# Performance work log

Hardware: AMD Instinct MI355X
Metric: run time of the kernel (lower is better)

Reference implementation:

```python
import jax, jax.numpy as jnp
import numpy as np
import math

NUM_REG_TOKENS = 0  # encoder.num_register_tokens
EPS = 1e-12         # matches torch F.normalize eps


def _l2norm(x):
    # F.normalize(x, dim=-1): x / max(||x||, eps)
    n = jnp.sqrt(jnp.sum(x * x, axis=-1, keepdims=True))
    return x / jnp.maximum(n, EPS)


def setup_inputs() -> dict:
    key = jax.random.key(0)
    k1, k2 = jax.random.split(key)
    L, N, S, T, D = 3, 8, 4, 1370, 768  # 3 interested layers, T = 1 + 37^2 patches
    q_feats = jax.random.normal(k1, (L, N, T, D), dtype=jnp.float32)
    s_feats = jax.random.normal(k2, (L, N * S, T, D), dtype=jnp.float32)
    return {"q_feats": q_feats, "s_feats": s_feats}


def reference(q_feats, s_feats):
    # fuse_feature: mean over stacked interested layers
    xq = jnp.mean(q_feats, axis=0)   # [N, T, D]
    xs = jnp.mean(s_feats, axis=0)   # [N*S, T, D]
    N = xq.shape[0]
    Q = xq.shape[1] - 1 - NUM_REG_TOKENS
    side = int(math.isqrt(Q))
    # drop class (+register) tokens
    xq = xq[:, 1 + NUM_REG_TOKENS:, :]                 # [N, Q, D]
    xs = xs[:, 1 + NUM_REG_TOKENS:, :]                 # [N*S, Q, D]
    xs = xs.reshape(N, -1, xs.shape[-1])               # [N, S*Q, D]
    xq = _l2norm(xq)
    xs = _l2norm(xs)
    # cosine distance + 1-NN min over support tokens
    sim = jnp.einsum('nqd,nsd->nqs', xq, xs)           # [N, Q, S*Q]
    dist = jnp.min(1.0 - sim, axis=-1)                 # [N, Q]
    return dist.reshape(N, 1, side, side)
```

## Files before the change

### kernel.cpp

```cpp
#include <hip/hip_runtime.h>
#include <hip/hip_bf16.h>

typedef __attribute__((ext_vector_type(16))) float f32x16;
typedef __attribute__((ext_vector_type(8))) int i32x8;

#define T_TOK 1370
#define DDIM  768
#define SCV   1369
#define SCP   1408
#define MQP   1536
#define NB    8
#define NSLAB 32
#define NST   44
#define NMT   6

#define MEMFENCE asm volatile("" ::: "memory")
#define BARRIER  do { __builtin_amdgcn_s_barrier(); MEMFENCE; } while (0)

#define GLOAD_LDS16(g, l)                                                     \
  __builtin_amdgcn_global_load_lds(                                           \
      (const __attribute__((address_space(1))) unsigned int*)(g),             \
      (__attribute__((address_space(3))) unsigned int*)(l), 16, 0, 0)

extern "C" __global__ __launch_bounds__(192) void prep_kernel(
    const float* __restrict__ src, unsigned char* __restrict__ dst,
    size_t lstride)
{
  const int row  = blockIdx.x;
  const int slab = blockIdx.y;
  const int t    = threadIdx.x;
  unsigned char* drow = dst + ((size_t)slab * gridDim.x + row) * DDIM;
  if (row >= SCV) {
    reinterpret_cast<unsigned int*>(drow)[t] = 0u;
    return;
  }
  const float* base = src + ((size_t)slab * T_TOK + row + 1) * DDIM;
  float4 a = reinterpret_cast<const float4*>(base)[t];
  float4 b = reinterpret_cast<const float4*>(base + lstride)[t];
  float4 c = reinterpret_cast<const float4*>(base + 2 * lstride)[t];
  const float k3 = 1.0f / 3.0f;
  float4 m;
  m.x = (a.x + b.x + c.x) * k3;
  m.y = (a.y + b.y + c.y) * k3;
  m.z = (a.z + b.z + c.z) * k3;
  m.w = (a.w + b.w + c.w) * k3;
  float ss = m.x * m.x + m.y * m.y + m.z * m.z + m.w * m.w;
  #pragma unroll
  for (int d = 1; d < 64; d <<= 1) ss += __shfl_xor(ss, d);
  __shared__ float wsum[3];
  if ((t & 63) == 0) wsum[t >> 6] = ss;
  __syncthreads();
  float tot = wsum[0] + wsum[1] + wsum[2];
  float rn = 1.0f / fmaxf(sqrtf(tot), 1e-12f);
  int pk = __builtin_amdgcn_cvt_pk_fp8_f32(m.x * rn, m.y * rn, 0, false);
  pk = __builtin_amdgcn_cvt_pk_fp8_f32(m.z * rn, m.w * rn, pk, true);
  reinterpret_cast<unsigned int*>(drow)[t] = (unsigned int)pk;
}

extern "C" __global__ __launch_bounds__(256, 2) void simmax_kernel(
    const unsigned char* __restrict__ xq,
    const unsigned char* __restrict__ xs,
    float* __restrict__ part)
{
  const int flat = blockIdx.x + NMT * (blockIdx.y + NST * blockIdx.z);
  const int swz  = (flat & 7) * (NMT * NST) + (flat >> 3);
  const int mt   = swz % NMT;
  const int st   = (swz / NMT) % NST;
  const int n    = swz / (NMT * NST);

  const int tid  = threadIdx.x;
  const int lane = tid & 63;
  const int w    = tid >> 6;
  const int wr   = w >> 1;
  const int wc   = w & 1;
  const int l31  = lane & 31;
  const int h    = lane >> 5;

  __shared__ unsigned char ring[3][24576];

  const int slab = st / 11;
  const int lt   = st - slab * 11;
  const unsigned char* gA = xq + ((size_t)n * MQP + (size_t)mt * 256) * DDIM;
  const unsigned char* gB =
      xs + ((size_t)(n * 4 + slab) * SCP + (size_t)lt * 128) * DDIM;

  int aoffg[4], aldso[4], boffg[2], bldso[2];
  #pragma unroll
  for (int i = 0; i < 4; ++i) {
    int c = w * 4 + i;
    int r = c * 16 + (lane >> 2);
    aoffg[i] = r * DDIM + (((lane & 3) ^ (r & 3)) << 4);
    aldso[i] = c * 1024;
  }
  #pragma unroll
  for (int i = 0; i < 2; ++i) {
    int c = w * 2 + i;
    int r = c * 16 + (lane >> 2);
    boffg[i] = r * DDIM + (((lane & 3) ^ (r & 3)) << 4);
    bldso[i] = 16384 + c * 1024;
  }

  int aoff[4], boff[2];
  #pragma unroll
  for (int mf = 0; mf < 4; ++mf) {
    int row = wr * 128 + mf * 32 + l31;
    aoff[mf] = row * 64 + ((((h << 1) ^ (row & 3))) << 4);
  }
  #pragma unroll
  for (int nf = 0; nf < 2; ++nf) {
    int row = wc * 64 + nf * 32 + l31;
    boff[nf] = 16384 + row * 64 + ((((h << 1) ^ (row & 3))) << 4);
  }

  f32x16 acc[4][2];
  {
    f32x16 zz = {0.f,0.f,0.f,0.f,0.f,0.f,0.f,0.f,
                 0.f,0.f,0.f,0.f,0.f,0.f,0.f,0.f};
    #pragma unroll
    for (int a = 0; a < 4; ++a)
      #pragma unroll
      for (int b = 0; b < 2; ++b) acc[a][b] = zz;
  }

  #define ISSUE(KT, RB)                                                      \
    do {                                                                     \
      const unsigned char* ga_ = gA + (KT) * 64;                             \
      const unsigned char* gb_ = gB + (KT) * 64;                             \
      unsigned char* lb_ = ring[RB];                                         \
      _Pragma("unroll") for (int i = 0; i < 4; ++i)                          \
        GLOAD_LDS16(ga_ + aoffg[i], lb_ + aldso[i]);                         \
      _Pragma("unroll") for (int i = 0; i < 2; ++i)                          \
        GLOAD_LDS16(gb_ + boffg[i], lb_ + bldso[i]);                         \
    } while (0)

  ISSUE(0, 0);
  ISSUE(1, 1);
  asm volatile("s_waitcnt vmcnt(6)" ::: "memory");
  BARRIER;

  for (int kt = 0; kt < 12; ++kt) {
    if (kt + 2 < 12) ISSUE(kt + 2, (kt + 2) % 3);

    const char* Cb = reinterpret_cast<const char*>(ring[kt % 3]);
    i32x8 bfr[2];
    #pragma unroll
    for (int nf = 0; nf < 2; ++nf) {
      int4 lo = *reinterpret_cast<const int4*>(Cb + boff[nf]);
      int4 hi = *reinterpret_cast<const int4*>(Cb + (boff[nf] ^ 16));
      bfr[nf] = i32x8{lo.x, lo.y, lo.z, lo.w, hi.x, hi.y, hi.z, hi.w};
    }
    __builtin_amdgcn_s_setprio(1);
    #pragma unroll
    for (int mf = 0; mf < 4; ++mf) {
      int4 lo = *reinterpret_cast<const int4*>(Cb + aoff[mf]);
      int4 hi = *reinterpret_cast<const int4*>(Cb + (aoff[mf] ^ 16));
      i32x8 af = i32x8{lo.x, lo.y, lo.z, lo.w, hi.x, hi.y, hi.z, hi.w};
      #pragma unroll
      for (int nf = 0; nf < 2; ++nf)
        acc[mf][nf] = __builtin_amdgcn_mfma_scale_f32_32x32x64_f8f6f4(
            af, bfr[nf], acc[mf][nf], 0, 0, 0, 127, 0, 127);
    }
    __builtin_amdgcn_s_setprio(0);

    if (kt < 10)       asm volatile("s_waitcnt vmcnt(6)" ::: "memory");
    else if (kt == 10) asm volatile("s_waitcnt vmcnt(0)" ::: "memory");
    if (kt < 11) BARRIER;
  }

  bool colv[2];
  #pragma unroll
  for (int nf = 0; nf < 2; ++nf)
    colv[nf] = (lt * 128 + wc * 64 + nf * 32 + l31) < SCV;

  float rm[4][16];
  #pragma unroll
  for (int mf = 0; mf < 4; ++mf)
    #pragma unroll
    for (int j = 0; j < 16; ++j) {
      float v = -1e30f;
      #pragma unroll
      for (int nf = 0; nf < 2; ++nf)
        if (colv[nf]) v = fmaxf(v, acc[mf][nf][j]);
      rm[mf][j] = v;
    }

  #pragma unroll
  for (int msk = 1; msk < 32; msk <<= 1)
    #pragma unroll
    for (int mf = 0; mf < 4; ++mf)
      #pragma unroll
      for (int j = 0; j < 16; ++j)
        rm[mf][j] = fmaxf(rm[mf][j], __shfl_xor(rm[mf][j], msk));

  __syncthreads();
  float* buf = reinterpret_cast<float*>(&ring[0][0]);
  if (l31 == 0) {
    #pragma unroll
    for (int mf = 0; mf < 4; ++mf)
      #pragma unroll
      for (int j = 0; j < 16; ++j) {
        int r = wr * 128 + mf * 32 + (j & 3) + 8 * (j >> 2) + 4 * h;
        buf[wc * 256 + r] = rm[mf][j];
      }
  }
  __syncthreads();
  if (tid < 256) {
    float v = fmaxf(buf[tid], buf[256 + tid]);
    part[((size_t)n * NST + st) * MQP + (size_t)mt * 256 + tid] = v;
  }
}

extern "C" __global__ void finalize_kernel(const float* __restrict__ part,
                                           float* __restrict__ out) {
  int i = blockIdx.x * 256 + threadIdx.x;
  if (i >= NB * SCV) return;
  int n = i / SCV, q = i - n * SCV;
  const float* p = part + (size_t)n * NST * MQP + q;
  float m = p[0];
  #pragma unroll 4
  for (int g = 1; g < NST; ++g) m = fmaxf(m, p[(size_t)g * MQP]);
  out[i] = 1.0f - m;
}

extern "C" void kernel_launch(void* const* d_in, const int* in_sizes, int n_in,
                              void* d_out, int out_size, void* d_ws, size_t ws_size,
                              hipStream_t stream) {
  const float* q_feats = (const float*)d_in[0];
  const float* s_feats = (const float*)d_in[1];
  float* out = (float*)d_out;

  char* ws = (char*)d_ws;
  const size_t xq_bytes = (size_t)NB * MQP * DDIM;
  const size_t xs_bytes = (size_t)NSLAB * SCP * DDIM;
  unsigned char* xq = (unsigned char*)ws;
  unsigned char* xs = (unsigned char*)(ws + xq_bytes);
  float* part       = (float*)(ws + xq_bytes + xs_bytes);

  prep_kernel<<<dim3(MQP, NB), 192, 0, stream>>>(
      q_feats, xq, (size_t)NB * T_TOK * DDIM);
  prep_kernel<<<dim3(SCP, NSLAB), 192, 0, stream>>>(
      s_feats, xs, (size_t)NSLAB * T_TOK * DDIM);
  simmax_kernel<<<dim3(NMT, NST, NB), 256, 0, stream>>>(xq, xs, part);
  finalize_kernel<<<dim3((NB * SCV + 255) / 256), 256, 0, stream>>>(part, out);
}
```

Baseline: 214.2 us.

## Switch simmax to 16x16x128 FP8 MFMA with 128x128 tiles and 8 waves

Restructures the similarity GEMM to use 16x16x128 scaled FP8 MFMA instead of 32x32x64. The block tile shrinks to 128 query rows by 128 support rows, with 8 waves per block and twice as many M tiles. The K step doubles to 128 bytes with an 8-way XOR swizzle, and the 3-stage ring becomes a double buffer with a full vmcnt(0) wait each iteration. The goal is more parallelism and smaller per-wave accumulators, but it lowers per-block reuse of A/B data and reduces load/compute overlap.

```diff
diff --git a/kernel.cpp b/kernel.cpp
--- a/kernel.cpp
+++ b/kernel.cpp
@@ -1,7 +1,7 @@
 #include <hip/hip_runtime.h>
 #include <hip/hip_bf16.h>
 
-typedef __attribute__((ext_vector_type(16))) float f32x16;
+typedef __attribute__((ext_vector_type(4))) float f32x4;
 typedef __attribute__((ext_vector_type(8))) int i32x8;
 
 #define T_TOK 1370
@@ -12,10 +12,11 @@
 #define NB    8
 #define NSLAB 32
 #define NST   44
-#define NMT   6
+#define NMT   12
 
 #define MEMFENCE asm volatile("" ::: "memory")
 #define BARRIER  do { __builtin_amdgcn_s_barrier(); MEMFENCE; } while (0)
+#define VMCNT0   asm volatile("s_waitcnt vmcnt(0)" ::: "memory")
 
 #define GLOAD_LDS16(g, l)                                                     \
   __builtin_amdgcn_global_load_lds(                                           \
@@ -57,7 +58,7 @@
   reinterpret_cast<unsigned int*>(drow)[t] = (unsigned int)pk;
 }
 
-extern "C" __global__ __launch_bounds__(256, 2) void simmax_kernel(
+extern "C" __global__ __launch_bounds__(512, 2) void simmax_kernel(
     const unsigned char* __restrict__ xq,
     const unsigned char* __restrict__ xs,
     float* __restrict__ part)
@@ -71,51 +72,44 @@
   const int tid  = threadIdx.x;
   const int lane = tid & 63;
   const int w    = tid >> 6;
-  const int wr   = w >> 1;
-  const int wc   = w & 1;
-  const int l31  = lane & 31;
-  const int h    = lane >> 5;
-
-  __shared__ unsigned char ring[3][24576];
+  const int wr   = w >> 2;
+  const int wcn  = w & 3;
+  const int l15  = lane & 15, l4 = lane >> 4;
+
+  __shared__ unsigned char dbuf[2][32768];
+  __shared__ float sfold[512];
 
   const int slab = st / 11;
   const int lt   = st - slab * 11;
-  const unsigned char* gA = xq + ((size_t)n * MQP + (size_t)mt * 256) * DDIM;
+  const unsigned char* gA = xq + ((size_t)n * MQP + (size_t)mt * 128) * DDIM;
   const unsigned char* gB =
       xs + ((size_t)(n * 4 + slab) * SCP + (size_t)lt * 128) * DDIM;
 
-  int aoffg[4], aldso[4], boffg[2], bldso[2];
-  #pragma unroll
-  for (int i = 0; i < 4; ++i) {
-    int c = w * 4 + i;
-    int r = c * 16 + (lane >> 2);
-    aoffg[i] = r * DDIM + (((lane & 3) ^ (r & 3)) << 4);
-    aldso[i] = c * 1024;
-  }
+  int goff[2], aldso[2], bldso[2];
   #pragma unroll
   for (int i = 0; i < 2; ++i) {
     int c = w * 2 + i;
-    int r = c * 16 + (lane >> 2);
-    boffg[i] = r * DDIM + (((lane & 3) ^ (r & 3)) << 4);
+    int r = c * 8 + (lane >> 3);
+    goff[i]  = r * DDIM + (((lane & 7) ^ (r & 7)) << 4);
+    aldso[i] = c * 1024;
     bldso[i] = 16384 + c * 1024;
   }
 
   int aoff[4], boff[2];
   #pragma unroll
   for (int mf = 0; mf < 4; ++mf) {
-    int row = wr * 128 + mf * 32 + l31;
-    aoff[mf] = row * 64 + ((((h << 1) ^ (row & 3))) << 4);
+    int row = wr * 64 + mf * 16 + l15;
+    aoff[mf] = row * 128 + ((((l4 << 1) ^ (row & 7))) << 4);
   }
   #pragma unroll
   for (int nf = 0; nf < 2; ++nf) {
-    int row = wc * 64 + nf * 32 + l31;
-    boff[nf] = 16384 + row * 64 + ((((h << 1) ^ (row & 3))) << 4);
-  }
-
-  f32x16 acc[4][2];
+    int row = wcn * 32 + nf * 16 + l15;
+    boff[nf] = 16384 + row * 128 + ((((l4 << 1) ^ (row & 7))) << 4);
+  }
+
+  f32x4 acc[4][2];
   {
-    f32x16 zz = {0.f,0.f,0.f,0.f,0.f,0.f,0.f,0.f,
-                 0.f,0.f,0.f,0.f,0.f,0.f,0.f,0.f};
+    f32x4 zz = {0.f, 0.f, 0.f, 0.f};
     #pragma unroll
     for (int a = 0; a < 4; ++a)
       #pragma unroll
@@ -124,59 +118,59 @@
 
   #define ISSUE(KT, RB)                                                      \
     do {                                                                     \
-      const unsigned char* ga_ = gA + (KT) * 64;                             \
-      const unsigned char* gb_ = gB + (KT) * 64;                             \
-      unsigned char* lb_ = ring[RB];                                         \
-      _Pragma("unroll") for (int i = 0; i < 4; ++i)                          \
-        GLOAD_LDS16(ga_ + aoffg[i], lb_ + aldso[i]);                         \
+      const unsigned char* ga_ = gA + (KT) * 128;                            \
+      const unsigned char* gb_ = gB + (KT) * 128;                            \
+      unsigned char* lb_ = dbuf[RB];                                         \
       _Pragma("unroll") for (int i = 0; i < 2; ++i)                          \
-        GLOAD_LDS16(gb_ + boffg[i], lb_ + bldso[i]);                         \
+        GLOAD_LDS16(ga_ + goff[i], lb_ + aldso[i]);                          \
+      _Pragma("unroll") for (int i = 0; i < 2; ++i)                          \
+        GLOAD_LDS16(gb_ + goff[i], lb_ + bldso[i]);                          \
     } while (0)
 
+  #define READ_FRAG(PTR, OFF, DST)                                           \
+    do {                                                                     \
+      int4 lo_ = *reinterpret_cast<const int4*>((PTR) + (OFF));              \
+      int4 hi_ = *reinterpret_cast<const int4*>((PTR) + ((OFF) ^ 16));       \
+      DST = i32x8{lo_.x, lo_.y, lo_.z, lo_.w, hi_.x, hi_.y, hi_.z, hi_.w};   \
+    } while (0)
+
   ISSUE(0, 0);
-  ISSUE(1, 1);
-  asm volatile("s_waitcnt vmcnt(6)" ::: "memory");
+  VMCNT0;
   BARRIER;
 
-  for (int kt = 0; kt < 12; ++kt) {
-    if (kt + 2 < 12) ISSUE(kt + 2, (kt + 2) % 3);
-
-    const char* Cb = reinterpret_cast<const char*>(ring[kt % 3]);
-    i32x8 bfr[2];
-    #pragma unroll
-    for (int nf = 0; nf < 2; ++nf) {
-      int4 lo = *reinterpret_cast<const int4*>(Cb + boff[nf]);
-      int4 hi = *reinterpret_cast<const int4*>(Cb + (boff[nf] ^ 16));
-      bfr[nf] = i32x8{lo.x, lo.y, lo.z, lo.w, hi.x, hi.y, hi.z, hi.w};
-    }
+  for (int kt = 0; kt < 6; ++kt) {
+    if (kt + 1 < 6) ISSUE(kt + 1, (kt + 1) & 1);
+
+    const char* Cb = reinterpret_cast<const char*>(dbuf[kt & 1]);
+    i32x8 bfr[2], af[4];
+    #pragma unroll
+    for (int nf = 0; nf < 2; ++nf) READ_FRAG(Cb, boff[nf], bfr[nf]);
+    #pragma unroll
+    for (int mf = 0; mf < 4; ++mf) READ_FRAG(Cb, aoff[mf], af[mf]);
+
     __builtin_amdgcn_s_setprio(1);
     #pragma unroll
-    for (int mf = 0; mf < 4; ++mf) {
-      int4 lo = *reinterpret_cast<const int4*>(Cb + aoff[mf]);
-      int4 hi = *reinterpret_cast<const int4*>(Cb + (aoff[mf] ^ 16));
-      i32x8 af = i32x8{lo.x, lo.y, lo.z, lo.w, hi.x, hi.y, hi.z, hi.w};
+    for (int mf = 0; mf < 4; ++mf)
       #pragma unroll
       for (int nf = 0; nf < 2; ++nf)
-        acc[mf][nf] = __builtin_amdgcn_mfma_scale_f32_32x32x64_f8f6f4(
-            af, bfr[nf], acc[mf][nf], 0, 0, 0, 127, 0, 127);
-    }
+        acc[mf][nf] = __builtin_amdgcn_mfma_scale_f32_16x16x128_f8f6f4(
+            af[mf], bfr[nf], acc[mf][nf], 0, 0, 0, 127, 0, 127);
     __builtin_amdgcn_s_setprio(0);
 
-    if (kt < 10)       asm volatile("s_waitcnt vmcnt(6)" ::: "memory");
-    else if (kt == 10) asm volatile("s_waitcnt vmcnt(0)" ::: "memory");
-    if (kt < 11) BARRIER;
+    if (kt + 1 < 6) VMCNT0;
+    if (kt < 5) BARRIER;
   }
 
   bool colv[2];
   #pragma unroll
   for (int nf = 0; nf < 2; ++nf)
-    colv[nf] = (lt * 128 + wc * 64 + nf * 32 + l31) < SCV;
-
-  float rm[4][16];
+    colv[nf] = (lt * 128 + wcn * 32 + nf * 16 + l15) < SCV;
+
+  float rm[4][4];
   #pragma unroll
   for (int mf = 0; mf < 4; ++mf)
     #pragma unroll
-    for (int j = 0; j < 16; ++j) {
+    for (int j = 0; j < 4; ++j) {
       float v = -1e30f;
       #pragma unroll
       for (int nf = 0; nf < 2; ++nf)
@@ -185,28 +179,28 @@
     }
 
   #pragma unroll
-  for (int msk = 1; msk < 32; msk <<= 1)
+  for (int msk = 1; msk < 16; msk <<= 1)
     #pragma unroll
     for (int mf = 0; mf < 4; ++mf)
       #pragma unroll
-      for (int j = 0; j < 16; ++j)
+      for (int j = 0; j < 4; ++j)
         rm[mf][j] = fmaxf(rm[mf][j], __shfl_xor(rm[mf][j], msk));
 
   __syncthreads();
-  float* buf = reinterpret_cast<float*>(&ring[0][0]);
-  if (l31 == 0) {
+  if (l15 == 0) {
     #pragma unroll
     for (int mf = 0; mf < 4; ++mf)
       #pragma unroll
-      for (int j = 0; j < 16; ++j) {
-        int r = wr * 128 + mf * 32 + (j & 3) + 8 * (j >> 2) + 4 * h;
-        buf[wc * 256 + r] = rm[mf][j];
+      for (int j = 0; j < 4; ++j) {
+        int r = wr * 64 + mf * 16 + l4 * 4 + j;
+        sfold[wcn * 128 + r] = rm[mf][j];
       }
   }
   __syncthreads();
-  if (tid < 256) {
-    float v = fmaxf(buf[tid], buf[256 + tid]);
-    part[((size_t)n * NST + st) * MQP + (size_t)mt * 256 + tid] = v;
+  if (tid < 128) {
+    float v = fmaxf(fmaxf(sfold[tid], sfold[128 + tid]),
+                    fmaxf(sfold[256 + tid], sfold[384 + tid]));
+    part[((size_t)n * NST + st) * MQP + (size_t)mt * 128 + tid] = v;
   }
 }
 
@@ -240,6 +234,6 @@
       q_feats, xq, (size_t)NB * T_TOK * DDIM);
   prep_kernel<<<dim3(SCP, NSLAB), 192, 0, stream>>>(
       s_feats, xs, (size_t)NSLAB * T_TOK * DDIM);
-  simmax_kernel<<<dim3(NMT, NST, NB), 256, 0, stream>>>(xq, xs, part);
+  simmax_kernel<<<dim3(NMT, NST, NB), 512, 0, stream>>>(xq, xs, part);
   finalize_kernel<<<dim3((NB * SCV + 255) / 256), 256, 0, stream>>>(part, out);
 }
```

Result: faster. 199.2 us (-7.0%).
